# Optimization experiments

Measured on AMD Instinct MI355X. Metric: run time of the kernel, lower is better.

## Reference

```python
import jax, jax.numpy as jnp
import numpy as np

B, N, C = 8, 1025, 1024
H = 8
D = C // H  # 128
LORA = 16
TOK = 1024

def setup_inputs() -> dict:
    key = jax.random.key(0)
    ks = jax.random.split(key, 16)
    s = 0.02
    return {
        "x": jax.random.normal(ks[0], (B, N, C), jnp.float32),
        "style_k": jax.random.normal(ks[1], (B, N, C), jnp.float32),
        "style_v": jax.random.normal(ks[2], (B, N, C), jnp.float32),
        "W_qkv": jax.random.normal(ks[3], (C, 3 * C), jnp.float32) * s,
        "W_proj": jax.random.normal(ks[4], (C, C), jnp.float32) * s,
        "b_proj": jnp.zeros((C,), jnp.float32),
        "ak": jax.random.normal(ks[5], (TOK, LORA), jnp.float32) * s,
        "bk": jax.random.normal(ks[6], (LORA, C), jnp.float32) * s,
        "av": jax.random.normal(ks[7], (TOK, LORA), jnp.float32) * s,
        "bv": jax.random.normal(ks[8], (LORA, C), jnp.float32) * s,
        "W1": jax.random.normal(ks[9], (C, C // 4), jnp.float32) * s,
        "b1": jnp.zeros((C // 4,), jnp.float32),
        "W2": jax.random.normal(ks[10], (C // 4, 1), jnp.float32) * s,
        "b2": jnp.zeros((1,), jnp.float32),
    }

def reference(x, style_k, style_v, W_qkv, W_proj, b_proj, ak, bk, av, bv, W1, b1, W2, b2):
    Bx, Nx, Cx = x.shape
    # cls-token gating MLP over transposed patch tokens: cp has shape [B, C, N-1], N-1 == C
    cls_token = x[:, :1, :]                         # [B,1,C]
    cp = jnp.transpose(x[:, 1:, :], (0, 2, 1))      # [B,C,N-1]
    h = jax.nn.relu(cp @ W1 + b1)                   # [B,C,C//4]
    attn_w = jax.nn.sigmoid(h @ W2 + b2)            # [B,C,1]
    attn_w = attn_w[..., 0][:, None, :]             # [B,1,C]
    weighted_cls = cls_token * attn_w               # [B,1,C]

    qkv = (x @ W_qkv).reshape(Bx, Nx, 3, H, D)
    q, k, v = qkv[:, :, 0], qkv[:, :, 1], qkv[:, :, 2]  # each [B,N,H,D]

    tokens_k = ak @ bk                              # [TOK, C] (TOK == C)
    tokens_v = av @ bv
    lora_k = (style_k @ tokens_k.T).reshape(Bx, Nx, H, D)
    lora_v = (style_v @ tokens_v.T).reshape(Bx, Nx, H, D)

    kk = k + lora_k
    vv = v + lora_v
    scale = D ** -0.5  # xformers default softmax scale
    scores = jnp.einsum('bqhd,bkhd->bhqk', q, kk) * scale
    attn = jax.nn.softmax(scores, axis=-1)
    out = jnp.einsum('bhqk,bkhd->bqhd', attn, vv).reshape(Bx, Nx, Cx)
    out = out @ W_proj + b_proj

    x_return = jnp.concatenate([out[:, :1, :] + weighted_cls, out[:, 1:, :]], axis=1)
    return (x_return, vv)
```

## Files before the change

kernel.cpp:

```cpp
#include <hip/hip_runtime.h>
#include <hip/hip_bf16.h>
#include <stdint.h>

#define B_ 8
#define N_ 1025
#define C_ 1024
#define H_ 8
#define D_ 128
#define TOK_ 1024
#define LORA_ 16
#define M_ 8200
#define NPAD_ 1032

using bf16x8 = __attribute__((ext_vector_type(8))) short;
using f32x4  = __attribute__((ext_vector_type(4))) float;
typedef unsigned short u16;

__device__ __forceinline__ u16 f2bf(float f) {
    union { float f; unsigned u; } v; v.f = f;
    unsigned r = v.u + 0x7fffu + ((v.u >> 16) & 1u);
    return (u16)(r >> 16);
}

__device__ __forceinline__ unsigned cvt_pk_bf16(float lo, float hi) {
    unsigned r;
    asm("v_cvt_pk_bf16_f32 %0, %1, %2" : "=v"(r) : "v"(lo), "v"(hi));
    return r;
}

__device__ __forceinline__ void gload16(const u16* g, u16* l) {
    __builtin_amdgcn_global_load_lds(
        (const __attribute__((address_space(1))) void*)g,
        (__attribute__((address_space(3))) void*)l, 16, 0, 0);
}

__device__ __forceinline__ int xcd_swz(int bid, int nwg) {
    int cpx = nwg >> 3;
    return (bid & 7) * cpx + (bid >> 3);
}

__global__ __launch_bounds__(256) void cast3_kernel(
    const float* __restrict__ x, const float* __restrict__ sk, const float* __restrict__ sv,
    u16* __restrict__ xb, u16* __restrict__ skb, u16* __restrict__ svb)
{
    const float* in = blockIdx.y == 0 ? x : (blockIdx.y == 1 ? sk : sv);
    u16* out = blockIdx.y == 0 ? xb : (blockIdx.y == 1 ? skb : svb);
    size_t i = (size_t)blockIdx.x * 256 + threadIdx.x;
    float4 a = *((const float4*)in + i * 2);
    float4 b = *((const float4*)in + i * 2 + 1);
    bf16x8 v;
    v[0] = (short)f2bf(a.x); v[1] = (short)f2bf(a.y);
    v[2] = (short)f2bf(a.z); v[3] = (short)f2bf(a.w);
    v[4] = (short)f2bf(b.x); v[5] = (short)f2bf(b.y);
    v[6] = (short)f2bf(b.z); v[7] = (short)f2bf(b.w);
    *(bf16x8*)(out + i * 8) = v;
}

__global__ __launch_bounds__(256) void padcast16_kernel(
    const float* __restrict__ ak, const float* __restrict__ av,
    u16* __restrict__ akp, u16* __restrict__ avp)
{
    const float* in = blockIdx.y ? av : ak;
    u16* out = blockIdx.y ? avp : akp;
    int i = blockIdx.x * 256 + threadIdx.x;
    int t = i >> 4, l = i & 15;
    out[(size_t)t * 32 + l] = f2bf(in[i]);
    out[(size_t)t * 32 + 16 + l] = 0;
}

__global__ __launch_bounds__(256) void castb_kernel(
    const float* __restrict__ bk, const float* __restrict__ bv,
    u16* __restrict__ bkb, u16* __restrict__ bvb)
{
    const float* in = blockIdx.y ? bv : bk;
    u16* out = blockIdx.y ? bvb : bkb;
    int i = blockIdx.x * 256 + threadIdx.x;
    out[i] = f2bf(in[i]);
}

__global__ __launch_bounds__(256) void lora16_mfma(
    const u16* __restrict__ skb, const u16* __restrict__ svb,
    const u16* __restrict__ bkb, const u16* __restrict__ bvb,
    u16* __restrict__ sk16p, u16* __restrict__ sv16p)
{
    const u16* sb = blockIdx.y ? svb : skb;
    const u16* bb = blockIdx.y ? bvb : bkb;
    u16* op = blockIdx.y ? sv16p : sk16p;
    const int lane = threadIdx.x & 63, wid = threadIdx.x >> 6;
    const int base = blockIdx.x * 64 + wid * 16;
    int ma = base + (lane & 15); if (ma > M_ - 1) ma = M_ - 1;
    const int l = lane & 15;
    const u16* arow = sb + (size_t)ma * C_ + (lane >> 4) * 8;
    const u16* brow = bb + (size_t)l * C_ + (lane >> 4) * 8;
    f32x4 acc = {0.f, 0.f, 0.f, 0.f};
#pragma unroll
    for (int k0 = 0; k0 < C_; k0 += 32) {
        bf16x8 af = *(const bf16x8*)(arow + k0);
        bf16x8 bf = *(const bf16x8*)(brow + k0);
        acc = __builtin_amdgcn_mfma_f32_16x16x32_bf16(af, bf, acc, 0, 0, 0);
    }
#pragma unroll
    for (int r = 0; r < 4; ++r) {
        int m = base + (lane >> 4) * 4 + r; if (m > M_ - 1) m = M_ - 1;
        op[(size_t)m * 32 + l] = f2bf(acc[r]);
        op[(size_t)m * 32 + 16 + l] = 0;
    }
}

__global__ __launch_bounds__(256) void wt_kernel(
    const float* __restrict__ in, u16* __restrict__ out, int K, int Nw)
{
    __shared__ float t[32][33];
    int n0 = blockIdx.x * 32, k0 = blockIdx.y * 32;
    int tx = threadIdx.x & 31, ty = threadIdx.x >> 5;
#pragma unroll
    for (int yy = 0; yy < 32; yy += 8)
        t[ty + yy][tx] = in[(size_t)(k0 + ty + yy) * Nw + n0 + tx];
    __syncthreads();
#pragma unroll
    for (int yy = 0; yy < 32; yy += 8)
        out[(size_t)(n0 + ty + yy) * K + k0 + tx] = f2bf(t[tx][ty + yy]);
}

__global__ __launch_bounds__(256) void xt_kernel(
    const float* __restrict__ x, u16* __restrict__ xT)
{
    __shared__ float tb[32][33];
    int t0 = blockIdx.x * 32, c0 = blockIdx.y * 32, b = blockIdx.z;
    int tx = threadIdx.x & 31, ty = threadIdx.x >> 5;
#pragma unroll
    for (int yy = 0; yy < 32; yy += 8)
        tb[ty + yy][tx] = x[((size_t)b * N_ + 1 + t0 + ty + yy) * C_ + c0 + tx];
    __syncthreads();
#pragma unroll
    for (int yy = 0; yy < 32; yy += 8)
        xT[((size_t)b * 1024 + c0 + ty + yy) * 1024 + t0 + tx] = f2bf(tb[tx][ty + yy]);
}

__global__ __launch_bounds__(256) void vvt_kernel(
    const float* __restrict__ vv, u16* __restrict__ vvT)
{
    __shared__ float t[32][33];
    int n0 = blockIdx.x * 32, d0 = blockIdx.y * 32, bh = blockIdx.z;
    int b = bh >> 3, h = bh & 7;
    int tx = threadIdx.x & 31, ty = threadIdx.x >> 5;
#pragma unroll
    for (int yy = 0; yy < 32; yy += 8) {
        int n = n0 + ty + yy; if (n > 1024) n = 1024;
        t[ty + yy][tx] = vv[((size_t)(b * N_) + n) * C_ + h * D_ + d0 + tx];
    }
    __syncthreads();
#pragma unroll
    for (int yy = 0; yy < 32; yy += 8) {
        int n = n0 + tx;
        if (n < NPAD_)
            vvT[((size_t)bh * D_ + d0 + ty + yy) * NPAD_ + n] = f2bf(t[tx][ty + yy]);
    }
}

__device__ __forceinline__ void stage_tile(
    const u16* __restrict__ base, int row0, int maxrow,
    u16* lds, int k0, int lane, int wid)
{
#pragma unroll
    for (int j = 0; j < 4; ++j) {
        int i = wid * 4 + j;
        int p = i * 1024 + 16 * lane;
        int row = p >> 7, cb = p & 127;
        int cbs = cb ^ ((row & 7) << 4);
        int gr = row0 + row; if (gr > maxrow) gr = maxrow;
        gload16(base + (size_t)gr * 1024 + k0 + (cbs >> 1), lds + i * 512);
    }
}

__device__ __forceinline__ void gemm_pass(
    const u16* __restrict__ A, const u16* __restrict__ Bt, int row0, int nb0,
    u16* As, u16* Bs, f32x4 acc[4][4],
    const int lane, const int wid, const int wr, const int wc)
{
    for (int k0 = 0; k0 < 1024; k0 += 64) {
        __syncthreads();
        stage_tile(A,  row0, M_ - 1,    As, k0, lane, wid);
        stage_tile(Bt, nb0,  (1 << 30), Bs, k0, lane, wid);
        __syncthreads();
#pragma unroll
        for (int ks = 0; ks < 2; ++ks) {
            bf16x8 af[4], bfr[4];
#pragma unroll
            for (int mi = 0; mi < 4; ++mi) {
                int r = wr * 64 + mi * 16 + (lane & 15);
                int byte = (r * 128 + ks * 64 + (lane >> 4) * 16) ^ ((r & 7) << 4);
                af[mi] = *(const bf16x8*)((const char*)As + byte);
            }
#pragma unroll
            for (int ni = 0; ni < 4; ++ni) {
                int r = wc * 64 + ni * 16 + (lane & 15);
                int byte = (r * 128 + ks * 64 + (lane >> 4) * 16) ^ ((r & 7) << 4);
                bfr[ni] = *(const bf16x8*)((const char*)Bs + byte);
            }
#pragma unroll
            for (int mi = 0; mi < 4; ++mi)
#pragma unroll
                for (int ni = 0; ni < 4; ++ni)
                    acc[mi][ni] = __builtin_amdgcn_mfma_f32_16x16x32_bf16(
                        af[mi], bfr[ni], acc[mi][ni], 0, 0, 0);
        }
    }
}

__global__ __launch_bounds__(256) void se_gemm(
    const u16* __restrict__ xT, const u16* __restrict__ W1T,
    const float* __restrict__ b1, const float* __restrict__ W2,
    const float* __restrict__ b2, const float* __restrict__ x,
    float* __restrict__ wcls)
{
    __shared__ u16 As[8192], Bs[8192];
    __shared__ float red[128];
    const int tid = threadIdx.x, lane = tid & 63, wid = tid >> 6;
    const int wr = wid >> 1, wc = wid & 1;
    const int row0 = blockIdx.x * 128;
    if (tid < 128) red[tid] = 0.f;
    const f32x4 FZ = {0.f, 0.f, 0.f, 0.f};

#pragma unroll
    for (int pass = 0; pass < 2; ++pass) {
        f32x4 acc[4][4];
#pragma unroll
        for (int mi = 0; mi < 4; ++mi)
#pragma unroll
            for (int ni = 0; ni < 4; ++ni) acc[mi][ni] = FZ;
        gemm_pass(xT, W1T, row0, pass * 128, As, Bs, acc, lane, wid, wr, wc);
#pragma unroll
        for (int mi = 0; mi < 4; ++mi) {
#pragma unroll
            for (int r = 0; r < 4; ++r) {
                float v = 0.f;
#pragma unroll
                for (int ni = 0; ni < 4; ++ni) {
                    int j = pass * 128 + wc * 64 + ni * 16 + (lane & 15);
                    float h = acc[mi][ni][r] + b1[j];
                    v += fmaxf(h, 0.f) * W2[j];
                }
#pragma unroll
                for (int off = 1; off < 16; off <<= 1) v += __shfl_xor(v, off);
                if ((lane & 15) == 0)
                    atomicAdd(&red[wr * 64 + mi * 16 + (lane >> 4) * 4 + r], v);
            }
        }
    }
    __syncthreads();
    if (tid < 128) {
        int row = row0 + tid;
        int b = row >> 10, c = row & 1023;
        float aw = 1.f / (1.f + expf(-(red[tid] + b2[0])));
        wcls[row] = x[(size_t)b * N_ * C_ + c] * aw;
    }
}

__global__ __launch_bounds__(256) void qkv_gemm(
    const u16* __restrict__ xb, const u16* __restrict__ WqkvT,
    const u16* __restrict__ sk16p, const u16* __restrict__ sv16p,
    const u16* __restrict__ akp, const u16* __restrict__ avp,
    u16* __restrict__ qb, u16* __restrict__ kkb, float* __restrict__ vvout)
{
    __shared__ u16 As[8192], Bs[8192];
    const int tid = threadIdx.x, lane = tid & 63, wid = tid >> 6;
    const int wr = wid >> 1, wc = wid & 1;
    const int swz = xcd_swz(blockIdx.x, 65 * 24);
    const int row0 = (swz / 24) * 128;
    const int ct = swz % 24, region = ct >> 3;
    const int creg = (ct & 7) * 128;
    const f32x4 FZ = {0.f, 0.f, 0.f, 0.f};
    f32x4 acc[4][4];
#pragma unroll
    for (int mi = 0; mi < 4; ++mi)
#pragma unroll
        for (int ni = 0; ni < 4; ++ni) acc[mi][ni] = FZ;

    gemm_pass(xb, WqkvT, row0, ct * 128, As, Bs, acc, lane, wid, wr, wc);

    if (region >= 1) {
        const u16* a16 = (region == 1) ? sk16p : sv16p;
        const u16* b16 = (region == 1) ? akp : avp;
        bf16x8 af2[4], bf2v[4];
#pragma unroll
        for (int mi = 0; mi < 4; ++mi) {
            int gr = row0 + wr * 64 + mi * 16 + (lane & 15);
            if (gr > M_ - 1) gr = M_ - 1;
            af2[mi] = *(const bf16x8*)(a16 + (size_t)gr * 32 + (lane >> 4) * 8);
        }
#pragma unroll
        for (int ni = 0; ni < 4; ++ni) {
            int gc = creg + wc * 64 + ni * 16 + (lane & 15);
            bf2v[ni] = *(const bf16x8*)(b16 + (size_t)gc * 32 + (lane >> 4) * 8);
        }
#pragma unroll
        for (int mi = 0; mi < 4; ++mi)
#pragma unroll
            for (int ni = 0; ni < 4; ++ni)
                acc[mi][ni] = __builtin_amdgcn_mfma_f32_16x16x32_bf16(
                    af2[mi], bf2v[ni], acc[mi][ni], 0, 0, 0);
    }

#pragma unroll
    for (int mi = 0; mi < 4; ++mi) {
#pragma unroll
        for (int r = 0; r < 4; ++r) {
            int gr = row0 + wr * 64 + mi * 16 + (lane >> 4) * 4 + r;
            if (gr >= M_) continue;
#pragma unroll
            for (int ni = 0; ni < 4; ++ni) {
                int gc = creg + wc * 64 + ni * 16 + (lane & 15);
                float v = acc[mi][ni][r];
                if (region == 0)      qb [(size_t)gr * C_ + gc] = f2bf(v);
                else if (region == 1) kkb[(size_t)gr * C_ + gc] = f2bf(v);
                else                  vvout[(size_t)gr * C_ + gc] = v;
            }
        }
    }
}

__global__ __launch_bounds__(256) void proj_gemm(
    const u16* __restrict__ ob, const u16* __restrict__ WprojT,
    const float* __restrict__ bias, const float* __restrict__ wcls,
    float* __restrict__ outp)
{
    __shared__ u16 As[8192], Bs[8192];
    const int tid = threadIdx.x, lane = tid & 63, wid = tid >> 6;
    const int wr = wid >> 1, wc = wid & 1;
    const int swz = xcd_swz(blockIdx.x, 65 * 8);
    const int row0 = (swz / 8) * 128;
    const int ct = swz % 8;
    const f32x4 FZ = {0.f, 0.f, 0.f, 0.f};
    f32x4 acc[4][4];
#pragma unroll
    for (int mi = 0; mi < 4; ++mi)
#pragma unroll
        for (int ni = 0; ni < 4; ++ni) acc[mi][ni] = FZ;

    gemm_pass(ob, WprojT, row0, ct * 128, As, Bs, acc, lane, wid, wr, wc);

#pragma unroll
    for (int mi = 0; mi < 4; ++mi) {
#pragma unroll
        for (int r = 0; r < 4; ++r) {
            int gr = row0 + wr * 64 + mi * 16 + (lane >> 4) * 4 + r;
            if (gr >= M_) continue;
#pragma unroll
            for (int ni = 0; ni < 4; ++ni) {
                int gc = ct * 128 + wc * 64 + ni * 16 + (lane & 15);
                float v = acc[mi][ni][r] + bias[gc];
                if (gr % N_ == 0) v += wcls[(gr / N_) * C_ + gc];
                outp[(size_t)gr * C_ + gc] = v;
            }
        }
    }
}

__device__ __forceinline__ void stageK(
    const u16* __restrict__ kbase, u16* Ksb, int kv0, int lane, int wid)
{
#pragma unroll
    for (int j = 0; j < 4; ++j) {
        int i = wid * 4 + j;
        int p = i * 1024 + 16 * lane;
        int row = p >> 8, cb = p & 255;
        int cbs = cb ^ ((row & 7) << 4);
        int n = kv0 + row; if (n > 1024) n = 1024;
        gload16(kbase + (size_t)n * C_ + (cbs >> 1), Ksb + i * 512);
    }
}
__device__ __forceinline__ void stageV(
    const u16* __restrict__ vbase, u16* Vsb, int kv0, int lane, int wid)
{
#pragma unroll
    for (int j = 0; j < 4; ++j) {
        int i = wid * 4 + j;
        int p = i * 1024 + 16 * lane;
        int row = p >> 7, cb = p & 127;
        int cbs = cb ^ ((row & 7) << 4);
        int st = kv0 + (cbs >> 1); if (st > NPAD_ - 8) st = NPAD_ - 8;
        gload16(vbase + (size_t)row * NPAD_ + st, Vsb + i * 512);
    }
}

__device__ __forceinline__ int psw(int pr, int colb) {
    return (pr * 128 + colb) ^ ((pr & 7) << 4) ^ ((pr & 8) << 2);
}

__global__ __launch_bounds__(256) void attn_kernel(
    const u16* __restrict__ qb, const u16* __restrict__ kkb,
    const u16* __restrict__ vvT, u16* __restrict__ ob)
{
    __shared__ u16 Ks[8192];
    __shared__ u16 Vs[8192];
    __shared__ u16 Ps[4096];
    const int tid = threadIdx.x, lane = tid & 63, wid = tid >> 6;
    const int swz = xcd_swz(blockIdx.x, 17 * 64);
    const int qt = swz % 17, bh = swz / 17, b = bh >> 3, h = bh & 7;
    const int n0q = qt * 64;
    const float C2 = 0.1275006182f;
    const float THR = 11.54f;
    const u16* kbase = kkb + (size_t)b * N_ * C_ + h * D_;
    const u16* vbase = vvT + (size_t)bh * D_ * NPAD_;

    bf16x8 qf[4];
    {
        int qrow = n0q + wid * 16 + (lane & 15); if (qrow > 1024) qrow = 1024;
        const u16* qbase = qb + (size_t)(b * N_ + qrow) * C_ + h * D_ + (lane >> 4) * 8;
#pragma unroll
        for (int ks = 0; ks < 4; ++ks) qf[ks] = *(const bf16x8*)(qbase + ks * 32);
    }

    const bf16x8 ones = {0x3F80, 0x3F80, 0x3F80, 0x3F80, 0x3F80, 0x3F80, 0x3F80, 0x3F80};
    float mrow[4];
    const f32x4 FZ = {0.f, 0.f, 0.f, 0.f};
    f32x4 of[8], lsacc = FZ;
#pragma unroll
    for (int r = 0; r < 4; ++r) mrow[r] = -3e38f;
#pragma unroll
    for (int ct = 0; ct < 8; ++ct) of[ct] = FZ;

    char* psb = (char*)Ps + wid * 2048;

    for (int t = 0; t < 17; ++t) {
        const int kv0 = t * 64;
        __syncthreads();
        stageK(kbase, Ks, kv0, lane, wid);
        stageV(vbase, Vs, kv0, lane, wid);
        __syncthreads();

        f32x4 s[4];
        __builtin_amdgcn_s_setprio(1);
#pragma unroll
        for (int jt = 0; jt < 4; ++jt) {
            f32x4 a = FZ;
#pragma unroll
            for (int ks = 0; ks < 4; ++ks) {
                int kvr = jt * 16 + (lane & 15);
                int byte = (kvr * 256 + ks * 64 + (lane >> 4) * 16) ^ ((kvr & 7) << 4);
                bf16x8 kf = *(const bf16x8*)((const char*)Ks + byte);
                a = __builtin_amdgcn_mfma_f32_16x16x32_bf16(qf[ks], kf, a, 0, 0, 0);
            }
            s[jt] = a * C2;
        }
        __builtin_amdgcn_s_setprio(0);
        if (t == 16) {
#pragma unroll
            for (int jt = 0; jt < 4; ++jt) {
                int kvglob = kv0 + jt * 16 + (lane & 15);
                if (kvglob > 1024) {
                    s[jt][0] = -3e38f; s[jt][1] = -3e38f;
                    s[jt][2] = -3e38f; s[jt][3] = -3e38f;
                }
            }
        }

        float rmax[4];
#pragma unroll
        for (int r = 0; r < 4; ++r)
            rmax[r] = fmaxf(fmaxf(s[0][r], s[1][r]), fmaxf(s[2][r], s[3][r]));
        float g = fmaxf(fmaxf(rmax[0], rmax[1]), fmaxf(rmax[2], rmax[3]));
#pragma unroll
        for (int off = 1; off < 16; off <<= 1) g = fmaxf(g, __shfl_xor(g, off));
        int need = 0;
#pragma unroll
        for (int r = 0; r < 4; ++r) need |= (g > mrow[r] + THR) ? 1 : 0;

        if (__any(need)) {
            float al[4];
#pragma unroll
            for (int r = 0; r < 4; ++r) {
                float t0 = rmax[r];
#pragma unroll
                for (int off = 1; off < 16; off <<= 1) t0 = fmaxf(t0, __shfl_xor(t0, off));
                float mn = fmaxf(mrow[r], t0);
                al[r] = exp2f(mrow[r] - mn);
                mrow[r] = mn;
            }
#pragma unroll
            for (int ct = 0; ct < 8; ++ct)
#pragma unroll
                for (int r = 0; r < 4; ++r) of[ct][r] *= al[r];
#pragma unroll
            for (int r = 0; r < 4; ++r) lsacc[r] *= al[r];
        }
#pragma unroll
        for (int jt = 0; jt < 4; ++jt)
#pragma unroll
            for (int r = 0; r < 4; ++r) s[jt][r] = exp2f(s[jt][r] - mrow[r]);

#pragma unroll
        for (int jt = 0; jt < 4; ++jt) {
            unsigned pk01 = cvt_pk_bf16(s[jt][0], s[jt][1]);
            unsigned pk23 = cvt_pk_bf16(s[jt][2], s[jt][3]);
            int colb = (jt * 16 + (lane & 15)) * 2;
            int pr0 = (lane >> 4) * 4;
            *(u16*)(psb + psw(pr0,     colb)) = (u16)pk01;
            *(u16*)(psb + psw(pr0 + 1, colb)) = (u16)(pk01 >> 16);
            *(u16*)(psb + psw(pr0 + 2, colb)) = (u16)pk23;
            *(u16*)(psb + psw(pr0 + 3, colb)) = (u16)(pk23 >> 16);
        }

        bf16x8 pa[2];
#pragma unroll
        for (int ks2 = 0; ks2 < 2; ++ks2) {
            int prr = lane & 15;
            pa[ks2] = *(const bf16x8*)(psb + psw(prr, ks2 * 64 + (lane >> 4) * 16));
        }

        __builtin_amdgcn_s_setprio(1);
        lsacc = __builtin_amdgcn_mfma_f32_16x16x32_bf16(pa[0], ones, lsacc, 0, 0, 0);
        lsacc = __builtin_amdgcn_mfma_f32_16x16x32_bf16(pa[1], ones, lsacc, 0, 0, 0);
#pragma unroll
        for (int ct = 0; ct < 8; ++ct)
#pragma unroll
            for (int ks2 = 0; ks2 < 2; ++ks2) {
                int d = ct * 16 + (lane & 15);
                int byte = (d * 128 + ks2 * 64 + (lane >> 4) * 16) ^ ((d & 7) << 4);
                bf16x8 vf = *(const bf16x8*)((const char*)Vs + byte);
                of[ct] = __builtin_amdgcn_mfma_f32_16x16x32_bf16(pa[ks2], vf, of[ct], 0, 0, 0);
            }
        __builtin_amdgcn_s_setprio(0);
    }

#pragma unroll
    for (int ct = 0; ct < 8; ++ct)
#pragma unroll
        for (int r = 0; r < 4; ++r) {
            int n = n0q + wid * 16 + (lane >> 4) * 4 + r;
            if (n <= 1024)
                ob[(size_t)(b * N_ + n) * C_ + h * D_ + ct * 16 + (lane & 15)] =
                    f2bf(of[ct][r] / lsacc[r]);
        }
}

extern "C" void kernel_launch(void* const* d_in, const int* in_sizes, int n_in,
                              void* d_out, int out_size, void* d_ws, size_t ws_size,
                              hipStream_t stream)
{
    const float* x       = (const float*)d_in[0];
    const float* style_k = (const float*)d_in[1];
    const float* style_v = (const float*)d_in[2];
    const float* W_qkv   = (const float*)d_in[3];
    const float* W_proj  = (const float*)d_in[4];
    const float* b_proj  = (const float*)d_in[5];
    const float* ak      = (const float*)d_in[6];
    const float* bk      = (const float*)d_in[7];
    const float* av      = (const float*)d_in[8];
    const float* bv      = (const float*)d_in[9];
    const float* W1      = (const float*)d_in[10];
    const float* b1      = (const float*)d_in[11];
    const float* W2      = (const float*)d_in[12];
    const float* b2      = (const float*)d_in[13];

    float* outp   = (float*)d_out;
    float* vv_out = outp + (size_t)M_ * C_;

    u16* WqkvT = (u16*)outp;
    u16* xbb   = WqkvT + (size_t)3072 * 1024;
    u16* W1T   = xbb + (size_t)M_ * C_;
    u16* akp   = W1T + (size_t)256 * 1024;
    u16* avp   = akp + 1024 * 32;
    u16* bkb   = avp + 1024 * 32;
    u16* bvb   = bkb + 16 * 1024;
    u16* sk16p = bvb + 16 * 1024;
    u16* sv16p = sk16p + (size_t)M_ * 32;

    u16* ws     = (u16*)d_ws;
    u16* qb     = ws;
    u16* kkb    = qb  + (size_t)M_ * C_;
    u16* obuf   = kkb + (size_t)M_ * C_;
    u16* vvT    = obuf + (size_t)M_ * C_;
    u16* WprojT = vvT + (size_t)B_ * H_ * D_ * NPAD_;
    float* wcls = (float*)(WprojT + (size_t)1024 * 1024);
    u16* skb = obuf;
    u16* svb = vvT;
    u16* xT  = qb;

    wt_kernel<<<dim3(96, 32), 256, 0, stream>>>(W_qkv, WqkvT, 1024, 3072);
    wt_kernel<<<dim3(32, 32), 256, 0, stream>>>(W_proj, WprojT, 1024, 1024);
    wt_kernel<<<dim3(8, 32), 256, 0, stream>>>(W1, W1T, 1024, 256);
    padcast16_kernel<<<dim3(64, 2), 256, 0, stream>>>(ak, av, akp, avp);
    castb_kernel<<<dim3(64, 2), 256, 0, stream>>>(bk, bv, bkb, bvb);
    cast3_kernel<<<dim3(4100, 3), 256, 0, stream>>>(x, style_k, style_v, xbb, skb, svb);
    xt_kernel<<<dim3(32, 32, 8), 256, 0, stream>>>(x, xT);
    se_gemm<<<dim3(64), 256, 0, stream>>>(xT, W1T, b1, W2, b2, x, wcls);
    lora16_mfma<<<dim3(129, 2), 256, 0, stream>>>(skb, svb, bkb, bvb, sk16p, sv16p);

    qkv_gemm<<<dim3(65 * 24), 256, 0, stream>>>(xbb, WqkvT, sk16p, sv16p, akp, avp,
                                                qb, kkb, vv_out);
    vvt_kernel<<<dim3(33, 4, 64), 256, 0, stream>>>(vv_out, vvT);
    attn_kernel<<<dim3(17 * 64), 256, 0, stream>>>(qb, kkb, vvT, obuf);
    proj_gemm<<<dim3(65 * 8), 256, 0, stream>>>(obuf, WprojT, b_proj, wcls, outp);
}
```

Measured before the change: 359.7 us.

## Split SE gemm across two blocks, fold softmax scale into Q, simplify K/V staging

The SE gating GEMM now runs its two column passes as separate blocks (grid 64x2), combining them through global atomics into a zeroed buffer, with a small finalize kernel applying sigmoid and the cls multiply. This doubles parallelism on a 64-block launch at the cost of an extra memset and kernel launch. The softmax scale is folded into Q when it is written out in the QKV GEMM, removing a multiply per score tile in attention. K/V staging in attention now uses precomputed, incrementally advanced pointers instead of recomputing addresses and clamps each tile. This drops the row clamps, so the last tile may read past the valid rows.

```diff
diff --git a/kernel.cpp b/kernel.cpp
--- a/kernel.cpp
+++ b/kernel.cpp
@@ -211,50 +211,51 @@
 __global__ __launch_bounds__(256) void se_gemm(
     const u16* __restrict__ xT, const u16* __restrict__ W1T,
     const float* __restrict__ b1, const float* __restrict__ W2,
-    const float* __restrict__ b2, const float* __restrict__ x,
-    float* __restrict__ wcls)
+    float* __restrict__ gred)
 {
     __shared__ u16 As[8192], Bs[8192];
     __shared__ float red[128];
     const int tid = threadIdx.x, lane = tid & 63, wid = tid >> 6;
     const int wr = wid >> 1, wc = wid & 1;
     const int row0 = blockIdx.x * 128;
+    const int pass = blockIdx.y;
     if (tid < 128) red[tid] = 0.f;
     const f32x4 FZ = {0.f, 0.f, 0.f, 0.f};
 
-#pragma unroll
-    for (int pass = 0; pass < 2; ++pass) {
-        f32x4 acc[4][4];
-#pragma unroll
-        for (int mi = 0; mi < 4; ++mi)
-#pragma unroll
-            for (int ni = 0; ni < 4; ++ni) acc[mi][ni] = FZ;
-        gemm_pass(xT, W1T, row0, pass * 128, As, Bs, acc, lane, wid, wr, wc);
-#pragma unroll
-        for (int mi = 0; mi < 4; ++mi) {
-#pragma unroll
-            for (int r = 0; r < 4; ++r) {
-                float v = 0.f;
-#pragma unroll
-                for (int ni = 0; ni < 4; ++ni) {
-                    int j = pass * 128 + wc * 64 + ni * 16 + (lane & 15);
-                    float h = acc[mi][ni][r] + b1[j];
-                    v += fmaxf(h, 0.f) * W2[j];
-                }
-#pragma unroll
-                for (int off = 1; off < 16; off <<= 1) v += __shfl_xor(v, off);
-                if ((lane & 15) == 0)
-                    atomicAdd(&red[wr * 64 + mi * 16 + (lane >> 4) * 4 + r], v);
-            }
+    f32x4 acc[4][4];
+#pragma unroll
+    for (int mi = 0; mi < 4; ++mi)
+#pragma unroll
+        for (int ni = 0; ni < 4; ++ni) acc[mi][ni] = FZ;
+    gemm_pass(xT, W1T, row0, pass * 128, As, Bs, acc, lane, wid, wr, wc);
+#pragma unroll
+    for (int mi = 0; mi < 4; ++mi) {
+#pragma unroll
+        for (int r = 0; r < 4; ++r) {
+            float v = 0.f;
+#pragma unroll
+            for (int ni = 0; ni < 4; ++ni) {
+                int j = pass * 128 + wc * 64 + ni * 16 + (lane & 15);
+                float h = acc[mi][ni][r] + b1[j];
+                v += fmaxf(h, 0.f) * W2[j];
+            }
+#pragma unroll
+            for (int off = 1; off < 16; off <<= 1) v += __shfl_xor(v, off);
+            if ((lane & 15) == 0)
+                atomicAdd(&red[wr * 64 + mi * 16 + (lane >> 4) * 4 + r], v);
         }
     }
     __syncthreads();
-    if (tid < 128) {
-        int row = row0 + tid;
-        int b = row >> 10, c = row & 1023;
-        float aw = 1.f / (1.f + expf(-(red[tid] + b2[0])));
-        wcls[row] = x[(size_t)b * N_ * C_ + c] * aw;
-    }
+    if (tid < 128) atomicAdd(&gred[row0 + tid], red[tid]);
+}
+
+__global__ __launch_bounds__(256) void se_fin(
+    const float* __restrict__ gred, const float* __restrict__ b2,
+    const float* __restrict__ x, float* __restrict__ wcls)
+{
+    int row = blockIdx.x * 256 + threadIdx.x;
+    int b = row >> 10, c = row & 1023;
+    wcls[row] = x[(size_t)b * N_ * C_ + c] / (1.f + expf(-(gred[row] + b2[0])));
 }
 
 __global__ __launch_bounds__(256) void qkv_gemm(
@@ -302,6 +303,7 @@
                     af2[mi], bf2v[ni], acc[mi][ni], 0, 0, 0);
     }
 
+    const float QSCALE = 0.1275006182f;
 #pragma unroll
     for (int mi = 0; mi < 4; ++mi) {
 #pragma unroll
@@ -312,7 +314,7 @@
             for (int ni = 0; ni < 4; ++ni) {
                 int gc = creg + wc * 64 + ni * 16 + (lane & 15);
                 float v = acc[mi][ni][r];
-                if (region == 0)      qb [(size_t)gr * C_ + gc] = f2bf(v);
+                if (region == 0)      qb [(size_t)gr * C_ + gc] = f2bf(v * QSCALE);
                 else if (region == 1) kkb[(size_t)gr * C_ + gc] = f2bf(v);
                 else                  vvout[(size_t)gr * C_ + gc] = v;
             }
@@ -357,33 +359,6 @@
     }
 }
 
-__device__ __forceinline__ void stageK(
-    const u16* __restrict__ kbase, u16* Ksb, int kv0, int lane, int wid)
-{
-#pragma unroll
-    for (int j = 0; j < 4; ++j) {
-        int i = wid * 4 + j;
-        int p = i * 1024 + 16 * lane;
-        int row = p >> 8, cb = p & 255;
-        int cbs = cb ^ ((row & 7) << 4);
-        int n = kv0 + row; if (n > 1024) n = 1024;
-        gload16(kbase + (size_t)n * C_ + (cbs >> 1), Ksb + i * 512);
-    }
-}
-__device__ __forceinline__ void stageV(
-    const u16* __restrict__ vbase, u16* Vsb, int kv0, int lane, int wid)
-{
-#pragma unroll
-    for (int j = 0; j < 4; ++j) {
-        int i = wid * 4 + j;
-        int p = i * 1024 + 16 * lane;
-        int row = p >> 7, cb = p & 127;
-        int cbs = cb ^ ((row & 7) << 4);
-        int st = kv0 + (cbs >> 1); if (st > NPAD_ - 8) st = NPAD_ - 8;
-        gload16(vbase + (size_t)row * NPAD_ + st, Vsb + i * 512);
-    }
-}
-
 __device__ __forceinline__ int psw(int pr, int colb) {
     return (pr * 128 + colb) ^ ((pr & 7) << 4) ^ ((pr & 8) << 2);
 }
@@ -399,7 +374,6 @@
     const int swz = xcd_swz(blockIdx.x, 17 * 64);
     const int qt = swz % 17, bh = swz / 17, b = bh >> 3, h = bh & 7;
     const int n0q = qt * 64;
-    const float C2 = 0.1275006182f;
     const float THR = 11.54f;
     const u16* kbase = kkb + (size_t)b * N_ * C_ + h * D_;
     const u16* vbase = vvT + (size_t)bh * D_ * NPAD_;
@@ -412,6 +386,14 @@
         for (int ks = 0; ks < 4; ++ks) qf[ks] = *(const bf16x8*)(qbase + ks * 32);
     }
 
+    const int rowK = wid * 16 + (lane >> 4);
+    const int cbsE = ((lane & 15) * 16) ^ ((rowK & 7) << 4);
+    const u16* kpe = kbase + (size_t)rowK * C_ + (cbsE >> 1);
+    const u16* kpo = kbase + (size_t)(rowK + 4) * C_ + ((cbsE ^ 64) >> 1);
+    const int rowV = wid * 32 + (lane >> 3);
+    const int cbsV = ((lane & 7) * 16) ^ ((rowV & 7) << 4);
+    const u16* vp = vbase + (size_t)rowV * NPAD_ + (cbsV >> 1);
+
     const bf16x8 ones = {0x3F80, 0x3F80, 0x3F80, 0x3F80, 0x3F80, 0x3F80, 0x3F80, 0x3F80};
     float mrow[4];
     const f32x4 FZ = {0.f, 0.f, 0.f, 0.f};
@@ -424,10 +406,16 @@
     char* psb = (char*)Ps + wid * 2048;
 
     for (int t = 0; t < 17; ++t) {
-        const int kv0 = t * 64;
         __syncthreads();
-        stageK(kbase, Ks, kv0, lane, wid);
-        stageV(vbase, Vs, kv0, lane, wid);
+        gload16(kpe,              Ks + (wid * 4 + 0) * 512);
+        gload16(kpo,              Ks + (wid * 4 + 1) * 512);
+        gload16(kpe + 8 * C_,     Ks + (wid * 4 + 2) * 512);
+        gload16(kpo + 8 * C_,     Ks + (wid * 4 + 3) * 512);
+        gload16(vp,               Vs + (wid * 4 + 0) * 512);
+        gload16(vp + 8 * NPAD_,   Vs + (wid * 4 + 1) * 512);
+        gload16(vp + 16 * NPAD_,  Vs + (wid * 4 + 2) * 512);
+        gload16(vp + 24 * NPAD_,  Vs + (wid * 4 + 3) * 512);
+        kpe += 64 * C_; kpo += 64 * C_; vp += 64;
         __syncthreads();
 
         f32x4 s[4];
@@ -442,13 +430,13 @@
                 bf16x8 kf = *(const bf16x8*)((const char*)Ks + byte);
                 a = __builtin_amdgcn_mfma_f32_16x16x32_bf16(qf[ks], kf, a, 0, 0, 0);
             }
-            s[jt] = a * C2;
+            s[jt] = a;
         }
         __builtin_amdgcn_s_setprio(0);
         if (t == 16) {
 #pragma unroll
             for (int jt = 0; jt < 4; ++jt) {
-                int kvglob = kv0 + jt * 16 + (lane & 15);
+                int kvglob = 1024 + jt * 16 + (lane & 15);
                 if (kvglob > 1024) {
                     s[jt][0] = -3e38f; s[jt][1] = -3e38f;
                     s[jt][2] = -3e38f; s[jt][3] = -3e38f;
@@ -574,6 +562,7 @@
     u16* vvT    = obuf + (size_t)M_ * C_;
     u16* WprojT = vvT + (size_t)B_ * H_ * D_ * NPAD_;
     float* wcls = (float*)(WprojT + (size_t)1024 * 1024);
+    float* gred = wcls + 8192;
     u16* skb = obuf;
     u16* svb = vvT;
     u16* xT  = qb;
@@ -585,7 +574,9 @@
     castb_kernel<<<dim3(64, 2), 256, 0, stream>>>(bk, bv, bkb, bvb);
     cast3_kernel<<<dim3(4100, 3), 256, 0, stream>>>(x, style_k, style_v, xbb, skb, svb);
     xt_kernel<<<dim3(32, 32, 8), 256, 0, stream>>>(x, xT);
-    se_gemm<<<dim3(64), 256, 0, stream>>>(xT, W1T, b1, W2, b2, x, wcls);
+    hipMemsetAsync(gred, 0, 8192 * sizeof(float), stream);
+    se_gemm<<<dim3(64, 2), 256, 0, stream>>>(xT, W1T, b1, W2, gred);
+    se_fin<<<dim3(32), 256, 0, stream>>>(gred, b2, x, wcls);
     lora16_mfma<<<dim3(129, 2), 256, 0, stream>>>(skb, svb, bkb, bvb, sk16p, sv16p);
 
     qkv_gemm<<<dim3(65 * 24), 256, 0, stream>>>(xbb, WqkvT, sk16p, sv16p, akp, avp,
```

Result: faster. 342.6 us (-4.8%).
